# Optimization experiments

Hardware: AMD Instinct MI355X
Metric: run time of the kernel (lower is better)

Reference implementation:

```python
import jax, jax.numpy as jnp
import numpy as np

B, S, U, H = 4, 2048, 1024, 16
DH = U // H  # head dim = 64
EPS = 1e-8


def setup_inputs() -> dict:
    key = jax.random.key(0)
    ks = jax.random.split(key, 7)
    scale = 1.0 / np.sqrt(U)
    return {
        "queries": jax.random.normal(ks[0], (B, S, U), jnp.float32),
        "keys": jax.random.normal(ks[1], (B, S, U), jnp.float32),
        "values": jax.random.normal(ks[2], (B, S, U), jnp.float32),
        "Wq": jax.random.normal(ks[3], (U, U), jnp.float32) * scale,
        "bq": jnp.zeros((U,), jnp.float32),
        "Wk": jax.random.normal(ks[4], (U, U), jnp.float32) * scale,
        "bk": jnp.zeros((U,), jnp.float32),
        "Wv": jax.random.normal(ks[5], (U, U), jnp.float32) * scale,
        "bv": jnp.zeros((U,), jnp.float32),
        "Wr": jax.random.normal(ks[6], (U, U), jnp.float32) * scale,
        "br": jnp.zeros((U,), jnp.float32),
        "gamma": jnp.ones((U,), jnp.float32),
        "beta": jnp.zeros((U,), jnp.float32),
    }


def reference(queries, keys, values, Wq, bq, Wk, bk, Wv, bv, Wr, br, gamma, beta):
    relu = jax.nn.relu
    Q = relu(queries @ Wq + bq)           # [B,S,U]
    K = relu(keys @ Wk + bk)
    V = relu(values @ Wv + bv)
    V_res = relu(values @ Wr + br)        # residual branch

    # split heads: tf.split(axis=2) + concat(axis=0) == per-head attention
    Qh = Q.reshape(B, S, H, DH)
    Kh = K.reshape(B, S, H, DH)
    Vh = V.reshape(B, S, H, DH)

    scores = jnp.einsum("bshd,bthd->bhst", Qh, Kh) / jnp.sqrt(jnp.float32(DH))
    w = jax.nn.softmax(scores, axis=-1)   # dropout keep_prob=1 -> identity
    out = jnp.einsum("bhst,bthd->bshd", w, Vh).reshape(B, S, U)

    out = relu(out + V_res)

    # manual LayerNorm (eps inside sqrt)
    mean = jnp.mean(out, axis=-1, keepdims=True)
    var = jnp.mean(jnp.square(out - mean), axis=-1, keepdims=True)
    normalized = (out - mean) / jnp.sqrt(var + EPS)
    return gamma * normalized + beta
```

## Files before the change

kernel.cpp:

```cpp
#include <hip/hip_runtime.h>

constexpr int B = 4, S = 2048, U = 1024, H = 16, DH = 64;
constexpr int MTOT = B * S;
constexpr int NT = S / 64;

using bf16   = __bf16;
using f32x4  = __attribute__((ext_vector_type(4))) float;
using f32x16 = __attribute__((ext_vector_type(16))) float;
using bf16x8 = __attribute__((ext_vector_type(8))) bf16;
using bf16x4 = __attribute__((ext_vector_type(4))) bf16;
using u32x4  = __attribute__((ext_vector_type(4))) unsigned int;

__device__ __forceinline__ void gload16(const bf16* g, bf16* l) {
  __builtin_amdgcn_global_load_lds(
      (const __attribute__((address_space(1))) unsigned int*)g,
      (__attribute__((address_space(3))) unsigned int*)l, 16, 0, 0);
}

__device__ __forceinline__ float fexp2(float x) {
#if __has_builtin(__builtin_amdgcn_exp2f)
  return __builtin_amdgcn_exp2f(x);
#else
  return __expf(x * 0.6931471805599453f);
#endif
}

__device__ __forceinline__ f32x16 mfma32(bf16x8 a, bf16x8 b, f32x16 c) {
  return __builtin_amdgcn_mfma_f32_32x32x16_bf16(a, b, c, 0, 0, 0);
}

__device__ __forceinline__ unsigned packbf(float a, float b) {
  union { bf16 h; unsigned short s; } ua, ub;
  ua.h = (bf16)a; ub.h = (bf16)b;
  return ((unsigned)ub.s << 16) | (unsigned)ua.s;
}

__device__ __forceinline__ size_t kpack_off(int M_, int col) {
  const int b = M_ >> 11, s = M_ & 2047;
  const int h = col >> 6, d = col & 63;
  const int bh = b * 16 + h;
  const int t = s >> 6, r64 = s & 63;
  const int tt = r64 >> 5, l31 = r64 & 31;
  const int ks = d >> 4, hi = (d >> 3) & 1, j = d & 7;
  const int ln = l31 + (hi << 5);
  return ((size_t)(bh * 32 + t) << 12) + (tt << 11) + (ks << 9) + (ln << 3) + j;
}

__device__ __forceinline__ size_t vpack_off(int M_, int col) {
  const int b = M_ >> 11, s = M_ & 2047;
  const int h = col >> 6, d = col & 63;
  const int bh = b * 16 + h;
  const int j = s & 7, hi = (s >> 3) & 1, ks = (s >> 4) & 3, t = s >> 6;
  const int dt = d >> 5, l31 = d & 31;
  const int ln = l31 + (hi << 5);
  return ((size_t)(bh * 32 + t) << 12) + (dt << 11) + (ks << 9) + (ln << 3) + j;
}

__global__ void transpose_w_kernel(const float* __restrict__ w0, const float* __restrict__ w1,
                                   const float* __restrict__ w2, const float* __restrict__ w3,
                                   bf16* __restrict__ t0, bf16* __restrict__ t1,
                                   bf16* __restrict__ t2, bf16* __restrict__ t3) {
  const float* W = blockIdx.z == 0 ? w0 : blockIdx.z == 1 ? w1 : blockIdx.z == 2 ? w2 : w3;
  bf16* Wt       = blockIdx.z == 0 ? t0 : blockIdx.z == 1 ? t1 : blockIdx.z == 2 ? t2 : t3;
  __shared__ float tile[32][33];
  const int k0 = blockIdx.x * 32, n0 = blockIdx.y * 32;
  const int tx = threadIdx.x, ty = threadIdx.y;
  for (int i = ty; i < 32; i += 8) tile[i][tx] = W[(size_t)(k0 + i) * U + n0 + tx];
  __syncthreads();
  for (int i = ty; i < 32; i += 8) Wt[(size_t)(n0 + i) * U + k0 + tx] = (bf16)tile[tx][i];
}

__global__ __launch_bounds__(256) void xcvt3_kernel(
    const float* __restrict__ x0, const float* __restrict__ x1, const float* __restrict__ x2,
    bf16* __restrict__ o0, bf16* __restrict__ o1, bf16* __restrict__ o2) {
  const float* x = blockIdx.z == 0 ? x0 : blockIdx.z == 1 ? x1 : x2;
  bf16* o       = blockIdx.z == 0 ? o0 : blockIdx.z == 1 ? o1 : o2;
  const size_t i = ((size_t)blockIdx.x * 256 + threadIdx.x) * 8;
  const float4 v0 = *reinterpret_cast<const float4*>(x + i);
  const float4 v1 = *reinterpret_cast<const float4*>(x + i + 4);
  bf16x8 r;
  r[0] = (bf16)v0.x; r[1] = (bf16)v0.y; r[2] = (bf16)v0.z; r[3] = (bf16)v0.w;
  r[4] = (bf16)v1.x; r[5] = (bf16)v1.y; r[6] = (bf16)v1.z; r[7] = (bf16)v1.w;
  *reinterpret_cast<bf16x8*>(o + i) = r;
}

__global__ __launch_bounds__(256) void gemm4_kernel(
    const bf16* __restrict__ Qc, const bf16* __restrict__ Kc, const bf16* __restrict__ Vc,
    const bf16* __restrict__ wqt, const bf16* __restrict__ wkt,
    const bf16* __restrict__ wvt, const bf16* __restrict__ wrt,
    const float* __restrict__ bq, const float* __restrict__ bk,
    const float* __restrict__ bv, const float* __restrict__ br,
    bf16* __restrict__ oq, bf16* __restrict__ okp,
    bf16* __restrict__ ovp, bf16* __restrict__ orr) {
  const int bid = blockIdx.x;
  const int wg = (bid & 7) * 256 + (bid >> 3);
  const int z = wg >> 9, rem = wg & 511;
  const int bm = (rem >> 3) * 128, bn = (rem & 7) * 128;

  const bf16* A     = z == 0 ? Qc : z == 1 ? Kc : Vc;
  const bf16* Wt    = z == 0 ? wqt : z == 1 ? wkt : z == 2 ? wvt : wrt;
  const float* bias = z == 0 ? bq : z == 1 ? bk : z == 2 ? bv : br;

  const int t = threadIdx.x, lane = t & 63, wid = t >> 6;
  const int wr = wid >> 1, wc = wid & 1;
  const int lm = lane & 15, hi = lane >> 4;

  __shared__ __align__(16) bf16 As[128][32];
  __shared__ __align__(16) bf16 Bs[128][32];

  f32x4 acc[4][4];
#pragma unroll
  for (int i = 0; i < 4; ++i)
#pragma unroll
    for (int j = 0; j < 4; ++j) acc[i][j] = f32x4{0.f, 0.f, 0.f, 0.f};

  const int srow = wid * 32 + (lane >> 2);
  const int scol = (((lane & 3) ^ ((lane >> 3) & 3))) * 8;
  const bf16* ga = A  + (size_t)(bm + srow) * U + scol;
  const bf16* gb = Wt + (size_t)(bn + srow) * U + scol;
  bf16* lA0 = &As[wid * 32][0];
  bf16* lA1 = &As[wid * 32 + 16][0];
  bf16* lB0 = &Bs[wid * 32][0];
  bf16* lB1 = &Bs[wid * 32 + 16][0];

  const int sw = (hi ^ ((lm >> 1) & 3)) * 8;

  for (int k0 = 0; k0 < U; k0 += 32) {
    __syncthreads();
    gload16(ga + k0, lA0);
    gload16(ga + (size_t)16 * U + k0, lA1);
    gload16(gb + k0, lB0);
    gload16(gb + (size_t)16 * U + k0, lB1);
    __syncthreads();

    bf16x8 a[4], bb[4];
#pragma unroll
    for (int mi = 0; mi < 4; ++mi)
      a[mi] = *reinterpret_cast<const bf16x8*>(&As[wr * 64 + mi * 16 + lm][sw]);
#pragma unroll
    for (int ni = 0; ni < 4; ++ni)
      bb[ni] = *reinterpret_cast<const bf16x8*>(&Bs[wc * 64 + ni * 16 + lm][sw]);
#pragma unroll
    for (int mi = 0; mi < 4; ++mi)
#pragma unroll
      for (int ni = 0; ni < 4; ++ni)
        acc[mi][ni] = __builtin_amdgcn_mfma_f32_16x16x32_bf16(a[mi], bb[ni], acc[mi][ni], 0, 0, 0);
  }

  const int mb = bm + wr * 64 + hi * 4;
  const int nb = bn + wc * 64 + lm;
  if (z == 1) {
#pragma unroll
    for (int ni = 0; ni < 4; ++ni) {
      const float bv_ = bias[nb + ni * 16];
#pragma unroll
      for (int mi = 0; mi < 4; ++mi)
#pragma unroll
        for (int r = 0; r < 4; ++r) {
          const float vv = fmaxf(acc[mi][ni][r] + bv_, 0.f);
          okp[kpack_off(mb + mi * 16 + r, nb + ni * 16)] = (bf16)vv;
        }
    }
  } else if (z == 2) {
#pragma unroll
    for (int ni = 0; ni < 4; ++ni) {
      const float bv_ = bias[nb + ni * 16];
#pragma unroll
      for (int mi = 0; mi < 4; ++mi)
#pragma unroll
        for (int r = 0; r < 4; ++r) {
          const float vv = fmaxf(acc[mi][ni][r] + bv_, 0.f);
          ovp[vpack_off(mb + mi * 16 + r, nb + ni * 16)] = (bf16)vv;
        }
    }
  } else {
    bf16* out = z == 0 ? oq : orr;
#pragma unroll
    for (int ni = 0; ni < 4; ++ni) {
      const float bv_ = bias[nb + ni * 16];
#pragma unroll
      for (int mi = 0; mi < 4; ++mi)
#pragma unroll
        for (int r = 0; r < 4; ++r) {
          const float vv = fmaxf(acc[mi][ni][r] + bv_, 0.f);
          out[(size_t)(mb + mi * 16 + r) * U + nb + ni * 16] = (bf16)vv;
        }
    }
  }
}

__global__ __launch_bounds__(256, 2) void attn_kernel(
    const bf16* __restrict__ Q, const bf16* __restrict__ Kp,
    const bf16* __restrict__ Vp, bf16* __restrict__ att) {
  const int bid = blockIdx.x;
  const int swz = (bid & 7) * 128 + (bid >> 3);
  const int bh = swz >> 4, qx = swz & 15;
  const int b = bh >> 4, h = bh & 15;
  const int tid = threadIdx.x;
  const int w = tid >> 6, lane = tid & 63;
  const int l31 = lane & 31, hi8 = lane >> 5;
  const int q0 = qx * 128 + w * 32;

  __shared__ __align__(16) bf16 kv[3][8192];

  const float qscale = 0.18033688011111606f;

  const bf16* qbase = Q + ((size_t)b * S + q0 + l31) * U + h * DH + hi8 * 8;
  bf16x8 qf[4];
#pragma unroll
  for (int ks = 0; ks < 4; ++ks) {
    bf16x8 v = *reinterpret_cast<const bf16x8*>(qbase + ks * 16);
#pragma unroll
    for (int j = 0; j < 8; ++j) v[j] = (bf16)((float)v[j] * qscale);
    qf[ks] = v;
  }

  bf16x8 onesf;
#pragma unroll
  for (int j = 0; j < 8; ++j) onesf[j] = (bf16)1.f;

  float m = 0.f;
  f32x16 o0 = (f32x16)0.f, o1 = (f32x16)0.f, osum = (f32x16)0.f;

  const bf16* kpb = Kp + (size_t)bh * 32 * 4096;
  const bf16* vpb = Vp + (size_t)bh * 32 * 4096;

  auto stagekv = [&](int buf, int t) {
    const size_t toff = (size_t)t * 4096;
    gload16(kpb + toff + tid * 8,        &kv[buf][tid * 8]);
    gload16(kpb + toff + 2048 + tid * 8, &kv[buf][2048 + tid * 8]);
    gload16(vpb + toff + tid * 8,        &kv[buf][4096 + tid * 8]);
    gload16(vpb + toff + 2048 + tid * 8, &kv[buf][6144 + tid * 8]);
  };

  stagekv(0, 0);
  stagekv(1, 1);
  asm volatile("s_waitcnt vmcnt(4)" ::: "memory");
  __builtin_amdgcn_s_barrier();
  __builtin_amdgcn_sched_barrier(0);

  int cur = 0;
  for (int t = 0; t < NT; ++t) {
    if (t + 2 < NT) {
      const int nb_ = cur + 2 >= 3 ? cur - 1 : cur + 2;
      stagekv(nb_, t + 2);
    }

    bf16x8 kf[2][4];
#pragma unroll
    for (int tt = 0; tt < 2; ++tt)
#pragma unroll
      for (int ks = 0; ks < 4; ++ks)
        kf[tt][ks] = *reinterpret_cast<const bf16x8*>(&kv[cur][(tt * 4 + ks) * 512 + lane * 8]);

    f32x16 s0 = (f32x16)(-m), s1 = (f32x16)(-m);
    __builtin_amdgcn_s_setprio(1);
#pragma unroll
    for (int ks = 0; ks < 4; ++ks) {
      s0 = mfma32(kf[0][ks], qf[ks], s0);
      s1 = mfma32(kf[1][ks], qf[ks], s1);
    }
    __builtin_amdgcn_s_setprio(0);

    bf16x8 vf[2][4];
#pragma unroll
    for (int dt = 0; dt < 2; ++dt)
#pragma unroll
      for (int ks = 0; ks < 4; ++ks)
        vf[dt][ks] = *reinterpret_cast<const bf16x8*>(&kv[cur][4096 + (dt * 4 + ks) * 512 + lane * 8]);

    float mx8[8];
#pragma unroll
    for (int i = 0; i < 8; ++i)
      mx8[i] = fmaxf(fmaxf(s0[i], s0[i + 8]), fmaxf(s1[i], s1[i + 8]));
    float mx = fmaxf(fmaxf(fmaxf(mx8[0], mx8[1]), fmaxf(mx8[2], mx8[3])),
                     fmaxf(fmaxf(mx8[4], mx8[5]), fmaxf(mx8[6], mx8[7])));
    {
      float ma = mx, mb_ = mx;
      asm("v_permlane32_swap_b32 %0, %1" : "+v"(ma), "+v"(mb_));
      mx = fmaxf(ma, mb_);
    }

    if (__any(mx > 8.f)) {
      const float d = fmaxf(mx, 0.f);
      const float f = fexp2(-d);
      m += d;
#pragma unroll
      for (int i = 0; i < 16; ++i) { s0[i] -= d; s1[i] -= d; }
#pragma unroll
      for (int r = 0; r < 16; ++r) {
        const float fr = __shfl(f, (r & 3) + 8 * (r >> 2) + 4 * hi8);
        o0[r] *= fr;
        o1[r] *= fr;
        osum[r] *= fr;
      }
    }

    unsigned wpk[16];
#pragma unroll
    for (int i = 0; i < 8; ++i) {
      wpk[i]     = packbf(fexp2(s0[2 * i]), fexp2(s0[2 * i + 1]));
      wpk[8 + i] = packbf(fexp2(s1[2 * i]), fexp2(s1[2 * i + 1]));
    }

    u32x4 fw[4];
#pragma unroll
    for (int fi = 0; fi < 4; ++fi) {
      unsigned a0 = wpk[fi * 4 + 0], b0 = wpk[fi * 4 + 2];
      unsigned a1 = wpk[fi * 4 + 1], b1 = wpk[fi * 4 + 3];
      asm("v_permlane32_swap_b32 %0, %1" : "+v"(a0), "+v"(b0));
      asm("v_permlane32_swap_b32 %0, %1" : "+v"(a1), "+v"(b1));
      fw[fi] = u32x4{a0, a1, b0, b1};
    }

    __builtin_amdgcn_s_setprio(1);
#pragma unroll
    for (int ks = 0; ks < 4; ++ks) {
      const bf16x8 pf = __builtin_bit_cast(bf16x8, fw[ks]);
      o0   = mfma32(pf, vf[0][ks], o0);
      o1   = mfma32(pf, vf[1][ks], o1);
      osum = mfma32(pf, onesf, osum);
    }
    __builtin_amdgcn_s_setprio(0);

    if (t + 1 < NT) {
      if (t + 2 < NT) asm volatile("s_waitcnt vmcnt(4)" ::: "memory");
      else            asm volatile("s_waitcnt vmcnt(0)" ::: "memory");
      __builtin_amdgcn_s_barrier();
      __builtin_amdgcn_sched_barrier(0);
    }
    cur = cur + 1 >= 3 ? 0 : cur + 1;
  }

  bf16* obase = att + ((size_t)b * S + q0) * U + h * DH + l31;
#pragma unroll
  for (int r = 0; r < 16; ++r) {
    const int row = (r & 3) + 8 * (r >> 2) + 4 * hi8;
    const float lr = 1.f / osum[r];
    obase[(size_t)row * U]      = (bf16)(o0[r] * lr);
    obase[(size_t)row * U + 32] = (bf16)(o1[r] * lr);
  }
}

__global__ __launch_bounds__(256) void ln_kernel(
    const bf16* __restrict__ att, const bf16* __restrict__ vres,
    const float* __restrict__ gamma, const float* __restrict__ beta,
    float* __restrict__ out) {
  const int row = blockIdx.x;
  const int t = threadIdx.x;
  const bf16* ar = att + (size_t)row * U;
  const bf16* vr = vres + (size_t)row * U;
  const bf16x4 av = *reinterpret_cast<const bf16x4*>(ar + t * 4);
  const bf16x4 vv = *reinterpret_cast<const bf16x4*>(vr + t * 4);
  float x[4];
  float sum = 0.f, sq = 0.f;
#pragma unroll
  for (int i = 0; i < 4; ++i) {
    x[i] = fmaxf((float)av[i] + (float)vv[i], 0.f);
    sum += x[i];
    sq += x[i] * x[i];
  }
#pragma unroll
  for (int mm = 1; mm < 64; mm <<= 1) {
    sum += __shfl_xor(sum, mm);
    sq  += __shfl_xor(sq, mm);
  }
  __shared__ float s1[4], s2[4];
  if ((t & 63) == 0) { s1[t >> 6] = sum; s2[t >> 6] = sq; }
  __syncthreads();
  sum = s1[0] + s1[1] + s1[2] + s1[3];
  sq  = s2[0] + s2[1] + s2[2] + s2[3];
  const float mean = sum * (1.f / U);
  float var = sq * (1.f / U) - mean * mean;
  var = fmaxf(var, 0.f);
  const float inv = rsqrtf(var + 1e-8f);
#pragma unroll
  for (int i = 0; i < 4; ++i) {
    const int c = t * 4 + i;
    out[(size_t)row * U + c] = gamma[c] * ((x[i] - mean) * inv) + beta[c];
  }
}

extern "C" void kernel_launch(void* const* d_in, const int* in_sizes, int n_in,
                              void* d_out, int out_size, void* d_ws, size_t ws_size,
                              hipStream_t stream) {
  const float* queries = (const float*)d_in[0];
  const float* keys    = (const float*)d_in[1];
  const float* values  = (const float*)d_in[2];
  const float* Wq = (const float*)d_in[3];
  const float* bq = (const float*)d_in[4];
  const float* Wk = (const float*)d_in[5];
  const float* bk = (const float*)d_in[6];
  const float* Wv = (const float*)d_in[7];
  const float* bv = (const float*)d_in[8];
  const float* Wr = (const float*)d_in[9];
  const float* br = (const float*)d_in[10];
  const float* gamma = (const float*)d_in[11];
  const float* beta  = (const float*)d_in[12];
  float* out = (float*)d_out;

  char* ws = (char*)d_ws;
  const size_t MB = 1024 * 1024;
  bf16* wqt  = (bf16*)(ws + 0 * MB);
  bf16* wkt  = (bf16*)(ws + 2 * MB);
  bf16* wvt  = (bf16*)(ws + 4 * MB);
  bf16* wrt  = (bf16*)(ws + 6 * MB);
  bf16* Qcvt = (bf16*)(ws + 8 * MB);
  bf16* Kcvt = (bf16*)(ws + 24 * MB);
  bf16* Vcvt = (bf16*)(ws + 40 * MB);
  bf16* Qb   = (bf16*)(ws + 56 * MB);
  bf16* Kp   = (bf16*)(ws + 72 * MB);
  bf16* Vp   = (bf16*)(ws + 88 * MB);
  bf16* attb = Qcvt;
  bf16* Rb   = Kcvt;

  transpose_w_kernel<<<dim3(32, 32, 4), dim3(32, 8), 0, stream>>>(
      Wq, Wk, Wv, Wr, wqt, wkt, wvt, wrt);
  xcvt3_kernel<<<dim3(4096, 1, 3), 256, 0, stream>>>(queries, keys, values, Qcvt, Kcvt, Vcvt);
  gemm4_kernel<<<dim3(2048), 256, 0, stream>>>(
      Qcvt, Kcvt, Vcvt, wqt, wkt, wvt, wrt, bq, bk, bv, br, Qb, Kp, Vp, Rb);
  attn_kernel<<<dim3(1024), 256, 0, stream>>>(Qb, Kp, Vp, attb);
  ln_kernel<<<dim3(MTOT), 256, 0, stream>>>(attb, Rb, gamma, beta, out);
}
```

Before: 233.9 us.

## Double-buffer GEMM LDS tiles and merge prep kernels into one launch

The projection GEMM gets two LDS buffers so the global-to-LDS load of the next K tile is issued before the MFMAs on the current tile. This replaces the two barriers per iteration with one waitcnt and barrier after the compute. Separately, the input-conversion and weight-transpose kernels are merged into a single launch to remove one launch and let the two jobs overlap. The cost is twice the GEMM LDS footprint, which may lower occupancy.

Result: slower. 247.8 us (+5.9%).

```diff
diff --git a/kernel.cpp b/kernel.cpp
--- a/kernel.cpp
+++ b/kernel.cpp
@@ -56,32 +56,38 @@
   return ((size_t)(bh * 32 + t) << 12) + (dt << 11) + (ks << 9) + (ln << 3) + j;
 }
 
-__global__ void transpose_w_kernel(const float* __restrict__ w0, const float* __restrict__ w1,
-                                   const float* __restrict__ w2, const float* __restrict__ w3,
-                                   bf16* __restrict__ t0, bf16* __restrict__ t1,
-                                   bf16* __restrict__ t2, bf16* __restrict__ t3) {
-  const float* W = blockIdx.z == 0 ? w0 : blockIdx.z == 1 ? w1 : blockIdx.z == 2 ? w2 : w3;
-  bf16* Wt       = blockIdx.z == 0 ? t0 : blockIdx.z == 1 ? t1 : blockIdx.z == 2 ? t2 : t3;
+__global__ __launch_bounds__(256) void prep_kernel(
+    const float* __restrict__ xq, const float* __restrict__ xk, const float* __restrict__ xv,
+    bf16* __restrict__ oq, bf16* __restrict__ ok, bf16* __restrict__ ov,
+    const float* __restrict__ w0, const float* __restrict__ w1,
+    const float* __restrict__ w2, const float* __restrict__ w3,
+    bf16* __restrict__ t0, bf16* __restrict__ t1,
+    bf16* __restrict__ t2, bf16* __restrict__ t3) {
   __shared__ float tile[32][33];
-  const int k0 = blockIdx.x * 32, n0 = blockIdx.y * 32;
-  const int tx = threadIdx.x, ty = threadIdx.y;
-  for (int i = ty; i < 32; i += 8) tile[i][tx] = W[(size_t)(k0 + i) * U + n0 + tx];
-  __syncthreads();
-  for (int i = ty; i < 32; i += 8) Wt[(size_t)(n0 + i) * U + k0 + tx] = (bf16)tile[tx][i];
-}
-
-__global__ __launch_bounds__(256) void xcvt3_kernel(
-    const float* __restrict__ x0, const float* __restrict__ x1, const float* __restrict__ x2,
-    bf16* __restrict__ o0, bf16* __restrict__ o1, bf16* __restrict__ o2) {
-  const float* x = blockIdx.z == 0 ? x0 : blockIdx.z == 1 ? x1 : x2;
-  bf16* o       = blockIdx.z == 0 ? o0 : blockIdx.z == 1 ? o1 : o2;
-  const size_t i = ((size_t)blockIdx.x * 256 + threadIdx.x) * 8;
-  const float4 v0 = *reinterpret_cast<const float4*>(x + i);
-  const float4 v1 = *reinterpret_cast<const float4*>(x + i + 4);
-  bf16x8 r;
-  r[0] = (bf16)v0.x; r[1] = (bf16)v0.y; r[2] = (bf16)v0.z; r[3] = (bf16)v0.w;
-  r[4] = (bf16)v1.x; r[5] = (bf16)v1.y; r[6] = (bf16)v1.z; r[7] = (bf16)v1.w;
-  *reinterpret_cast<bf16x8*>(o + i) = r;
+  const int bid = blockIdx.x;
+  const int t = threadIdx.x;
+  if (bid < 12288) {
+    const int z = bid >> 12, idx = bid & 4095;
+    const float* x = z == 0 ? xq : z == 1 ? xk : xv;
+    bf16* o       = z == 0 ? oq : z == 1 ? ok : ov;
+    const size_t i = ((size_t)idx * 256 + t) * 8;
+    const float4 v0 = *reinterpret_cast<const float4*>(x + i);
+    const float4 v1 = *reinterpret_cast<const float4*>(x + i + 4);
+    bf16x8 r;
+    r[0] = (bf16)v0.x; r[1] = (bf16)v0.y; r[2] = (bf16)v0.z; r[3] = (bf16)v0.w;
+    r[4] = (bf16)v1.x; r[5] = (bf16)v1.y; r[6] = (bf16)v1.z; r[7] = (bf16)v1.w;
+    *reinterpret_cast<bf16x8*>(o + i) = r;
+  } else {
+    const int wb = bid - 12288;
+    const int z = wb >> 10, ti = wb & 1023;
+    const float* W = z == 0 ? w0 : z == 1 ? w1 : z == 2 ? w2 : w3;
+    bf16* Wt       = z == 0 ? t0 : z == 1 ? t1 : z == 2 ? t2 : t3;
+    const int k0 = (ti & 31) * 32, n0 = (ti >> 5) * 32;
+    const int tx = t & 31, ty = t >> 5;
+    for (int i = ty; i < 32; i += 8) tile[i][tx] = W[(size_t)(k0 + i) * U + n0 + tx];
+    __syncthreads();
+    for (int i = ty; i < 32; i += 8) Wt[(size_t)(n0 + i) * U + k0 + tx] = (bf16)tile[tx][i];
+  }
 }
 
 __global__ __launch_bounds__(256) void gemm4_kernel(
@@ -105,8 +111,8 @@
   const int wr = wid >> 1, wc = wid & 1;
   const int lm = lane & 15, hi = lane >> 4;
 
-  __shared__ __align__(16) bf16 As[128][32];
-  __shared__ __align__(16) bf16 Bs[128][32];
+  __shared__ __align__(16) bf16 As[2][128][32];
+  __shared__ __align__(16) bf16 Bs[2][128][32];
 
   f32x4 acc[4][4];
 #pragma unroll
@@ -115,36 +121,46 @@
     for (int j = 0; j < 4; ++j) acc[i][j] = f32x4{0.f, 0.f, 0.f, 0.f};
 
   const int srow = wid * 32 + (lane >> 2);
-  const int scol = (((lane & 3) ^ ((lane >> 3) & 3))) * 8;
+  const int scol = ((lane & 3) ^ ((lane >> 3) & 3)) * 8;
   const bf16* ga = A  + (size_t)(bm + srow) * U + scol;
   const bf16* gb = Wt + (size_t)(bn + srow) * U + scol;
-  bf16* lA0 = &As[wid * 32][0];
-  bf16* lA1 = &As[wid * 32 + 16][0];
-  bf16* lB0 = &Bs[wid * 32][0];
-  bf16* lB1 = &Bs[wid * 32 + 16][0];
+
+  auto stage = [&](int buf, int k0) {
+    gload16(ga + k0,                  &As[buf][wid * 32][0]);
+    gload16(ga + (size_t)16 * U + k0, &As[buf][wid * 32 + 16][0]);
+    gload16(gb + k0,                  &Bs[buf][wid * 32][0]);
+    gload16(gb + (size_t)16 * U + k0, &Bs[buf][wid * 32 + 16][0]);
+  };
 
   const int sw = (hi ^ ((lm >> 1) & 3)) * 8;
 
-  for (int k0 = 0; k0 < U; k0 += 32) {
-    __syncthreads();
-    gload16(ga + k0, lA0);
-    gload16(ga + (size_t)16 * U + k0, lA1);
-    gload16(gb + k0, lB0);
-    gload16(gb + (size_t)16 * U + k0, lB1);
-    __syncthreads();
+  stage(0, 0);
+  asm volatile("s_waitcnt vmcnt(0)" ::: "memory");
+  __builtin_amdgcn_s_barrier();
+  __builtin_amdgcn_sched_barrier(0);
+
+  for (int k = 0; k < 32; ++k) {
+    const int cur = k & 1;
+    if (k + 1 < 32) stage(cur ^ 1, (k + 1) * 32);
 
     bf16x8 a[4], bb[4];
 #pragma unroll
     for (int mi = 0; mi < 4; ++mi)
-      a[mi] = *reinterpret_cast<const bf16x8*>(&As[wr * 64 + mi * 16 + lm][sw]);
+      a[mi] = *reinterpret_cast<const bf16x8*>(&As[cur][wr * 64 + mi * 16 + lm][sw]);
 #pragma unroll
     for (int ni = 0; ni < 4; ++ni)
-      bb[ni] = *reinterpret_cast<const bf16x8*>(&Bs[wc * 64 + ni * 16 + lm][sw]);
+      bb[ni] = *reinterpret_cast<const bf16x8*>(&Bs[cur][wc * 64 + ni * 16 + lm][sw]);
 #pragma unroll
     for (int mi = 0; mi < 4; ++mi)
 #pragma unroll
       for (int ni = 0; ni < 4; ++ni)
         acc[mi][ni] = __builtin_amdgcn_mfma_f32_16x16x32_bf16(a[mi], bb[ni], acc[mi][ni], 0, 0, 0);
+
+    if (k + 1 < 32) {
+      asm volatile("s_waitcnt vmcnt(0)" ::: "memory");
+      __builtin_amdgcn_s_barrier();
+      __builtin_amdgcn_sched_barrier(0);
+    }
   }
 
   const int mb = bm + wr * 64 + hi * 4;
@@ -414,9 +430,9 @@
   bf16* attb = Qcvt;
   bf16* Rb   = Kcvt;
 
-  transpose_w_kernel<<<dim3(32, 32, 4), dim3(32, 8), 0, stream>>>(
+  prep_kernel<<<dim3(16384), 256, 0, stream>>>(
+      queries, keys, values, Qcvt, Kcvt, Vcvt,
       Wq, Wk, Wv, Wr, wqt, wkt, wvt, wrt);
-  xcvt3_kernel<<<dim3(4096, 1, 3), 256, 0, stream>>>(queries, keys, values, Qcvt, Kcvt, Vcvt);
   gemm4_kernel<<<dim3(2048), 256, 0, stream>>>(
       Qcvt, Kcvt, Vcvt, wqt, wkt, wvt, wrt, bq, bk, bv, br, Qb, Kp, Vp, Rb);
   attn_kernel<<<dim3(1024), 256, 0, stream>>>(Qb, Kp, Vp, attb);
```
